# Kernel tuning notes

Measured on AMD Instinct MI355X. Metric: run time of the kernel, lower is better.

## Reference

```python
import jax, jax.numpy as jnp
import numpy as np

T, H, I = 8192, 2048, 768  # tokens, hidden_size, intermediate_size

def setup_inputs() -> dict:
    key = jax.random.key(0)
    k1, k2, k3, k4 = jax.random.split(key, 4)
    x = jax.random.normal(k1, (T, H), dtype=jnp.float32)
    # torch nn.Linear weight layout: [out_features, in_features]
    gate_w = jax.random.normal(k2, (I, H), dtype=jnp.float32) * (1.0 / np.sqrt(H))
    up_w = jax.random.normal(k3, (I, H), dtype=jnp.float32) * (1.0 / np.sqrt(H))
    down_w = jax.random.normal(k4, (H, I), dtype=jnp.float32) * (1.0 / np.sqrt(I))
    return {"x": x, "gate_w": gate_w, "up_w": up_w, "down_w": down_w}

def reference(x, gate_w, up_w, down_w):
    # fused SwiGLU MLP: down( silu(x @ gate^T) * (x @ up^T) )
    gate = jnp.einsum('th,ih->ti', x, gate_w)   # [T, I]
    up = jnp.einsum('th,ih->ti', x, up_w)       # [T, I]
    h = jax.nn.silu(gate) * up                   # [T, I]
    out = jnp.einsum('ti,hi->th', h, down_w)     # [T, H]
    return out
```

## Files before the change

kernel.cpp:

```cpp
#include <hip/hip_runtime.h>
#include <hip/hip_bf16.h>
#include <stdint.h>

#define T_DIM 8192
#define H_DIM 2048
#define I_DIM 768

typedef __bf16 bf16_t;
typedef bf16_t bf16x8 __attribute__((ext_vector_type(8)));
typedef bf16_t bf16x4 __attribute__((ext_vector_type(4)));
typedef float  f32x4  __attribute__((ext_vector_type(4)));

__device__ __forceinline__ void async_load16(const void* g, void* s) {
    __builtin_amdgcn_global_load_lds(
        (const __attribute__((address_space(1))) void*)g,
        (__attribute__((address_space(3))) void*)s, 16, 0, 0);
}

__global__ __launch_bounds__(256) void cvt_kernel(
    const float* __restrict__ X, const float* __restrict__ G,
    const float* __restrict__ U, const float* __restrict__ D,
    bf16_t* __restrict__ Xb, bf16_t* __restrict__ Gb,
    bf16_t* __restrict__ Ub, bf16_t* __restrict__ Db)
{
    const size_t N4X = (size_t)T_DIM * H_DIM / 4;
    const size_t N4W = (size_t)I_DIM * H_DIM / 4;
    const size_t total = N4X + 3 * N4W;
    for (size_t i = (size_t)blockIdx.x * blockDim.x + threadIdx.x; i < total;
         i += (size_t)gridDim.x * blockDim.x) {
        const float* s; bf16_t* d; size_t j = i;
        if (j < N4X) { s = X; d = Xb; }
        else {
            j -= N4X;
            if (j < N4W) { s = G; d = Gb; }
            else { j -= N4W;
                if (j < N4W) { s = U; d = Ub; }
                else { j -= N4W; s = D; d = Db; } }
        }
        float4 v = ((const float4*)s)[j];
        bf16x4 o;
        o[0] = (bf16_t)v.x; o[1] = (bf16_t)v.y; o[2] = (bf16_t)v.z; o[3] = (bf16_t)v.w;
        ((bf16x4*)d)[j] = o;
    }
}

__global__ __launch_bounds__(256) void gateup_kernel(
    const bf16_t* __restrict__ X,
    const bf16_t* __restrict__ Wg,
    const bf16_t* __restrict__ Wu,
    bf16_t* __restrict__ Hbuf)
{
    __shared__ __align__(16) bf16_t sA[128 * 32];
    __shared__ __align__(16) bf16_t sG[64 * 32];
    __shared__ __align__(16) bf16_t sU[64 * 32];

    const int tid   = threadIdx.x;
    const int lane  = tid & 63;
    const int wave  = tid >> 6;
    const int waveM = wave >> 1;
    const int waveN = wave & 1;
    const int quad  = lane >> 4;
    const int lrow  = lane & 15;

    const int blockM = blockIdx.x;
    const int blockN = blockIdx.y;

    f32x4 accG[4][2], accU[4][2];
#pragma unroll
    for (int i = 0; i < 4; i++)
#pragma unroll
        for (int j = 0; j < 2; j++) { accG[i][j] = (f32x4)(0.f); accU[i][j] = (f32x4)(0.f); }

    const int s0 = tid, s1 = tid + 256;
    const int rA0 = s0 >> 2, cA0 = (s0 & 3) * 8;
    const int rA1 = s1 >> 2, cA1 = (s1 & 3) * 8;
    const int rW  = tid >> 2, cW  = (tid & 3) * 8;

    const bf16_t* Ab = X  + (size_t)(blockM * 128) * H_DIM;
    const bf16_t* Gb = Wg + (size_t)(blockN * 64) * H_DIM;
    const bf16_t* Ub = Wu + (size_t)(blockN * 64) * H_DIM;

    for (int k0 = 0; k0 < H_DIM; k0 += 32) {
        async_load16(Ab + (size_t)rA0 * H_DIM + k0 + cA0, &sA[s0 * 8]);
        async_load16(Ab + (size_t)rA1 * H_DIM + k0 + cA1, &sA[s1 * 8]);
        async_load16(Gb + (size_t)rW  * H_DIM + k0 + cW,  &sG[tid * 8]);
        async_load16(Ub + (size_t)rW  * H_DIM + k0 + cW,  &sU[tid * 8]);
        __syncthreads();

        bf16x8 aF[4], gF[2], uF[2];
#pragma unroll
        for (int mi = 0; mi < 4; mi++) {
            int r = waveM * 64 + mi * 16 + lrow;
            aF[mi] = *(const bf16x8*)&sA[r * 32 + quad * 8];
        }
#pragma unroll
        for (int ni = 0; ni < 2; ni++) {
            int r = waveN * 32 + ni * 16 + lrow;
            gF[ni] = *(const bf16x8*)&sG[r * 32 + quad * 8];
            uF[ni] = *(const bf16x8*)&sU[r * 32 + quad * 8];
        }
        __syncthreads();

#pragma unroll
        for (int mi = 0; mi < 4; mi++)
#pragma unroll
            for (int ni = 0; ni < 2; ni++) {
                accG[mi][ni] = __builtin_amdgcn_mfma_f32_16x16x32_bf16(aF[mi], gF[ni], accG[mi][ni], 0, 0, 0);
                accU[mi][ni] = __builtin_amdgcn_mfma_f32_16x16x32_bf16(aF[mi], uF[ni], accU[mi][ni], 0, 0, 0);
            }
    }

#pragma unroll
    for (int mi = 0; mi < 4; mi++) {
#pragma unroll
        for (int ni = 0; ni < 2; ni++) {
#pragma unroll
            for (int r = 0; r < 4; r++) {
                int row = blockM * 128 + waveM * 64 + mi * 16 + quad * 4 + r;
                int col = blockN * 64 + waveN * 32 + ni * 16 + lrow;
                float g = accG[mi][ni][r];
                float u = accU[mi][ni][r];
                float h = (g / (1.f + __expf(-g))) * u;
                Hbuf[(size_t)row * I_DIM + col] = (bf16_t)h;
            }
        }
    }
}

__global__ __launch_bounds__(256) void down_kernel(
    const bf16_t* __restrict__ Hbuf,
    const bf16_t* __restrict__ Wd,
    float* __restrict__ Out)
{
    __shared__ __align__(16) bf16_t sA[128 * 32];
    __shared__ __align__(16) bf16_t sB[128 * 32];

    const int tid   = threadIdx.x;
    const int lane  = tid & 63;
    const int wave  = tid >> 6;
    const int waveM = wave >> 1;
    const int waveN = wave & 1;
    const int quad  = lane >> 4;
    const int lrow  = lane & 15;

    const int blockM = blockIdx.x;
    const int blockN = blockIdx.y;

    f32x4 acc[4][4];
#pragma unroll
    for (int i = 0; i < 4; i++)
#pragma unroll
        for (int j = 0; j < 4; j++) acc[i][j] = (f32x4)(0.f);

    const int s0 = tid, s1 = tid + 256;
    const int rA0 = s0 >> 2, cA0 = (s0 & 3) * 8;
    const int rA1 = s1 >> 2, cA1 = (s1 & 3) * 8;

    const bf16_t* Ab = Hbuf + (size_t)(blockM * 128) * I_DIM;
    const bf16_t* Bb = Wd   + (size_t)(blockN * 128) * I_DIM;

    for (int k0 = 0; k0 < I_DIM; k0 += 32) {
        async_load16(Ab + (size_t)rA0 * I_DIM + k0 + cA0, &sA[s0 * 8]);
        async_load16(Ab + (size_t)rA1 * I_DIM + k0 + cA1, &sA[s1 * 8]);
        async_load16(Bb + (size_t)rA0 * I_DIM + k0 + cA0, &sB[s0 * 8]);
        async_load16(Bb + (size_t)rA1 * I_DIM + k0 + cA1, &sB[s1 * 8]);
        __syncthreads();

        bf16x8 aF[4], bF[4];
#pragma unroll
        for (int mi = 0; mi < 4; mi++) {
            int r = waveM * 64 + mi * 16 + lrow;
            aF[mi] = *(const bf16x8*)&sA[r * 32 + quad * 8];
        }
#pragma unroll
        for (int ni = 0; ni < 4; ni++) {
            int r = waveN * 64 + ni * 16 + lrow;
            bF[ni] = *(const bf16x8*)&sB[r * 32 + quad * 8];
        }
        __syncthreads();

#pragma unroll
        for (int mi = 0; mi < 4; mi++)
#pragma unroll
            for (int ni = 0; ni < 4; ni++)
                acc[mi][ni] = __builtin_amdgcn_mfma_f32_16x16x32_bf16(aF[mi], bF[ni], acc[mi][ni], 0, 0, 0);
    }

#pragma unroll
    for (int mi = 0; mi < 4; mi++) {
#pragma unroll
        for (int ni = 0; ni < 4; ni++) {
#pragma unroll
            for (int r = 0; r < 4; r++) {
                int row = blockM * 128 + waveM * 64 + mi * 16 + quad * 4 + r;
                int col = blockN * 128 + waveN * 64 + ni * 16 + lrow;
                Out[(size_t)row * H_DIM + col] = acc[mi][ni][r];
            }
        }
    }
}

extern "C" void kernel_launch(void* const* d_in, const int* in_sizes, int n_in,
                              void* d_out, int out_size, void* d_ws, size_t ws_size,
                              hipStream_t stream) {
    const float* x  = (const float*)d_in[0];
    const float* gw = (const float*)d_in[1];
    const float* uw = (const float*)d_in[2];
    const float* dw = (const float*)d_in[3];
    float* out = (float*)d_out;

    bf16_t* xb = (bf16_t*)d_ws;
    bf16_t* gb = xb + (size_t)T_DIM * H_DIM;
    bf16_t* ub = gb + (size_t)I_DIM * H_DIM;
    bf16_t* db = ub + (size_t)I_DIM * H_DIM;
    bf16_t* hb = db + (size_t)I_DIM * H_DIM;

    cvt_kernel<<<2048, 256, 0, stream>>>(x, gw, uw, dw, xb, gb, ub, db);
    gateup_kernel<<<dim3(T_DIM / 128, I_DIM / 64), 256, 0, stream>>>(xb, gb, ub, hb);
    down_kernel<<<dim3(T_DIM / 128, H_DIM / 128), 256, 0, stream>>>(hb, db, out);
}
```

Before: 230.5 us.

## Double-buffer LDS tiles with prefetch and XOR-swizzle layout in both GEMMs

Both GEMM kernels now use two shared-memory buffers, issuing async global-to-LDS loads for the next K tile before computing the current one. Manual vmcnt waits and raw barriers replace the two __syncthreads per iteration. Global columns are XOR-swizzled into LDS and reads use matching precomputed offsets, to cut bank conflicts on fragment loads. This doubles LDS use per block, which may lower occupancy, and depends on the hand-written waitcnt ordering being correct.

```diff
diff --git a/kernel.cpp b/kernel.cpp
--- a/kernel.cpp
+++ b/kernel.cpp
@@ -44,15 +44,16 @@
     }
 }
 
+
 __global__ __launch_bounds__(256) void gateup_kernel(
     const bf16_t* __restrict__ X,
     const bf16_t* __restrict__ Wg,
     const bf16_t* __restrict__ Wu,
     bf16_t* __restrict__ Hbuf)
 {
-    __shared__ __align__(16) bf16_t sA[128 * 32];
-    __shared__ __align__(16) bf16_t sG[64 * 32];
-    __shared__ __align__(16) bf16_t sU[64 * 32];
+    __shared__ __align__(16) bf16_t sA[2][128 * 32];
+    __shared__ __align__(16) bf16_t sG[2][64 * 32];
+    __shared__ __align__(16) bf16_t sU[2][64 * 32];
 
     const int tid   = threadIdx.x;
     const int lane  = tid & 63;
@@ -72,34 +73,56 @@
         for (int j = 0; j < 2; j++) { accG[i][j] = (f32x4)(0.f); accU[i][j] = (f32x4)(0.f); }
 
     const int s0 = tid, s1 = tid + 256;
-    const int rA0 = s0 >> 2, cA0 = (s0 & 3) * 8;
-    const int rA1 = s1 >> 2, cA1 = (s1 & 3) * 8;
-    const int rW  = tid >> 2, cW  = (tid & 3) * 8;
+    const int rA0 = s0 >> 2, cA0 = (((s0 & 3) ^ ((rA0 >> 1) & 3)) * 8);
+    const int rA1 = s1 >> 2, cA1 = (((s1 & 3) ^ ((rA1 >> 1) & 3)) * 8);
+    const int rW  = tid >> 2, cW  = (((tid & 3) ^ ((rW >> 1) & 3)) * 8);
 
     const bf16_t* Ab = X  + (size_t)(blockM * 128) * H_DIM;
-    const bf16_t* Gb = Wg + (size_t)(blockN * 64) * H_DIM;
-    const bf16_t* Ub = Wu + (size_t)(blockN * 64) * H_DIM;
-
+    const bf16_t* Gw = Wg + (size_t)(blockN * 64) * H_DIM;
+    const bf16_t* Uw = Wu + (size_t)(blockN * 64) * H_DIM;
+
+    int aOff[4], wOff[2];
+#pragma unroll
+    for (int mi = 0; mi < 4; mi++) {
+        int r = waveM * 64 + mi * 16 + lrow;
+        aOff[mi] = r * 32 + ((quad ^ ((r >> 1) & 3)) * 8);
+    }
+#pragma unroll
+    for (int ni = 0; ni < 2; ni++) {
+        int r = waveN * 32 + ni * 16 + lrow;
+        wOff[ni] = r * 32 + ((quad ^ ((r >> 1) & 3)) * 8);
+    }
+
+    async_load16(Ab + (size_t)rA0 * H_DIM + cA0, &sA[0][s0 * 8]);
+    async_load16(Ab + (size_t)rA1 * H_DIM + cA1, &sA[0][s1 * 8]);
+    async_load16(Gw + (size_t)rW  * H_DIM + cW,  &sG[0][tid * 8]);
+    async_load16(Uw + (size_t)rW  * H_DIM + cW,  &sU[0][tid * 8]);
+
+    int cur = 0;
     for (int k0 = 0; k0 < H_DIM; k0 += 32) {
-        async_load16(Ab + (size_t)rA0 * H_DIM + k0 + cA0, &sA[s0 * 8]);
-        async_load16(Ab + (size_t)rA1 * H_DIM + k0 + cA1, &sA[s1 * 8]);
-        async_load16(Gb + (size_t)rW  * H_DIM + k0 + cW,  &sG[tid * 8]);
-        async_load16(Ub + (size_t)rW  * H_DIM + k0 + cW,  &sU[tid * 8]);
-        __syncthreads();
+        __builtin_amdgcn_s_barrier();
+        if (k0 + 32 < H_DIM) {
+            const int nxt = cur ^ 1;
+            async_load16(Ab + (size_t)rA0 * H_DIM + (k0 + 32) + cA0, &sA[nxt][s0 * 8]);
+            async_load16(Ab + (size_t)rA1 * H_DIM + (k0 + 32) + cA1, &sA[nxt][s1 * 8]);
+            async_load16(Gw + (size_t)rW  * H_DIM + (k0 + 32) + cW,  &sG[nxt][tid * 8]);
+            async_load16(Uw + (size_t)rW  * H_DIM + (k0 + 32) + cW,  &sU[nxt][tid * 8]);
+            asm volatile("s_waitcnt vmcnt(4)" ::: "memory");
+        } else {
+            asm volatile("s_waitcnt vmcnt(0)" ::: "memory");
+        }
+        __builtin_amdgcn_s_barrier();
+        asm volatile("" ::: "memory");
 
         bf16x8 aF[4], gF[2], uF[2];
 #pragma unroll
-        for (int mi = 0; mi < 4; mi++) {
-            int r = waveM * 64 + mi * 16 + lrow;
-            aF[mi] = *(const bf16x8*)&sA[r * 32 + quad * 8];
-        }
+        for (int mi = 0; mi < 4; mi++)
+            aF[mi] = *(const bf16x8*)&sA[cur][aOff[mi]];
 #pragma unroll
         for (int ni = 0; ni < 2; ni++) {
-            int r = waveN * 32 + ni * 16 + lrow;
-            gF[ni] = *(const bf16x8*)&sG[r * 32 + quad * 8];
-            uF[ni] = *(const bf16x8*)&sU[r * 32 + quad * 8];
-        }
-        __syncthreads();
+            gF[ni] = *(const bf16x8*)&sG[cur][wOff[ni]];
+            uF[ni] = *(const bf16x8*)&sU[cur][wOff[ni]];
+        }
 
 #pragma unroll
         for (int mi = 0; mi < 4; mi++)
@@ -108,6 +131,7 @@
                 accG[mi][ni] = __builtin_amdgcn_mfma_f32_16x16x32_bf16(aF[mi], gF[ni], accG[mi][ni], 0, 0, 0);
                 accU[mi][ni] = __builtin_amdgcn_mfma_f32_16x16x32_bf16(aF[mi], uF[ni], accU[mi][ni], 0, 0, 0);
             }
+        cur ^= 1;
     }
 
 #pragma unroll
@@ -132,8 +156,8 @@
     const bf16_t* __restrict__ Wd,
     float* __restrict__ Out)
 {
-    __shared__ __align__(16) bf16_t sA[128 * 32];
-    __shared__ __align__(16) bf16_t sB[128 * 32];
+    __shared__ __align__(16) bf16_t sA[2][128 * 32];
+    __shared__ __align__(16) bf16_t sB[2][128 * 32];
 
     const int tid   = threadIdx.x;
     const int lane  = tid & 63;
@@ -153,37 +177,59 @@
         for (int j = 0; j < 4; j++) acc[i][j] = (f32x4)(0.f);
 
     const int s0 = tid, s1 = tid + 256;
-    const int rA0 = s0 >> 2, cA0 = (s0 & 3) * 8;
-    const int rA1 = s1 >> 2, cA1 = (s1 & 3) * 8;
+    const int rA0 = s0 >> 2, cA0 = (((s0 & 3) ^ ((rA0 >> 1) & 3)) * 8);
+    const int rA1 = s1 >> 2, cA1 = (((s1 & 3) ^ ((rA1 >> 1) & 3)) * 8);
 
     const bf16_t* Ab = Hbuf + (size_t)(blockM * 128) * I_DIM;
     const bf16_t* Bb = Wd   + (size_t)(blockN * 128) * I_DIM;
 
+    int aOff[4], bOff[4];
+#pragma unroll
+    for (int mi = 0; mi < 4; mi++) {
+        int r = waveM * 64 + mi * 16 + lrow;
+        aOff[mi] = r * 32 + ((quad ^ ((r >> 1) & 3)) * 8);
+    }
+#pragma unroll
+    for (int ni = 0; ni < 4; ni++) {
+        int r = waveN * 64 + ni * 16 + lrow;
+        bOff[ni] = r * 32 + ((quad ^ ((r >> 1) & 3)) * 8);
+    }
+
+    async_load16(Ab + (size_t)rA0 * I_DIM + cA0, &sA[0][s0 * 8]);
+    async_load16(Ab + (size_t)rA1 * I_DIM + cA1, &sA[0][s1 * 8]);
+    async_load16(Bb + (size_t)rA0 * I_DIM + cA0, &sB[0][s0 * 8]);
+    async_load16(Bb + (size_t)rA1 * I_DIM + cA1, &sB[0][s1 * 8]);
+
+    int cur = 0;
     for (int k0 = 0; k0 < I_DIM; k0 += 32) {
-        async_load16(Ab + (size_t)rA0 * I_DIM + k0 + cA0, &sA[s0 * 8]);
-        async_load16(Ab + (size_t)rA1 * I_DIM + k0 + cA1, &sA[s1 * 8]);
-        async_load16(Bb + (size_t)rA0 * I_DIM + k0 + cA0, &sB[s0 * 8]);
-        async_load16(Bb + (size_t)rA1 * I_DIM + k0 + cA1, &sB[s1 * 8]);
-        __syncthreads();
+        __builtin_amdgcn_s_barrier();
+        if (k0 + 32 < I_DIM) {
+            const int nxt = cur ^ 1;
+            async_load16(Ab + (size_t)rA0 * I_DIM + (k0 + 32) + cA0, &sA[nxt][s0 * 8]);
+            async_load16(Ab + (size_t)rA1 * I_DIM + (k0 + 32) + cA1, &sA[nxt][s1 * 8]);
+            async_load16(Bb + (size_t)rA0 * I_DIM + (k0 + 32) + cA0, &sB[nxt][s0 * 8]);
+            async_load16(Bb + (size_t)rA1 * I_DIM + (k0 + 32) + cA1, &sB[nxt][s1 * 8]);
+            asm volatile("s_waitcnt vmcnt(4)" ::: "memory");
+        } else {
+            asm volatile("s_waitcnt vmcnt(0)" ::: "memory");
+        }
+        __builtin_amdgcn_s_barrier();
+        asm volatile("" ::: "memory");
 
         bf16x8 aF[4], bF[4];
 #pragma unroll
-        for (int mi = 0; mi < 4; mi++) {
-            int r = waveM * 64 + mi * 16 + lrow;
-            aF[mi] = *(const bf16x8*)&sA[r * 32 + quad * 8];
-        }
-#pragma unroll
-        for (int ni = 0; ni < 4; ni++) {
-            int r = waveN * 64 + ni * 16 + lrow;
-            bF[ni] = *(const bf16x8*)&sB[r * 32 + quad * 8];
-        }
-        __syncthreads();
+        for (int mi = 0; mi < 4; mi++)
+            aF[mi] = *(const bf16x8*)&sA[cur][aOff[mi]];
+#pragma unroll
+        for (int ni = 0; ni < 4; ni++)
+            bF[ni] = *(const bf16x8*)&sB[cur][bOff[ni]];
 
 #pragma unroll
         for (int mi = 0; mi < 4; mi++)
 #pragma unroll
             for (int ni = 0; ni < 4; ni++)
                 acc[mi][ni] = __builtin_amdgcn_mfma_f32_16x16x32_bf16(aF[mi], bF[ni], acc[mi][ni], 0, 0, 0);
+        cur ^= 1;
     }
 
 #pragma unroll
```

After: 251.2 us. +9.0%, slower.

## Double K-tile depth to 64 with XOR-swizzled LDS layout in both GEMMs

Applied to the files above, without the earlier changes.

Both GEMM kernels now stage 64-wide K slices per iteration instead of 32, halving the number of barrier pairs and load rounds. The LDS layout uses an XOR swizzle of the 16-byte chunk index by row, so fragment reads avoid bank conflicts. Each staged tile feeds two MFMA sub-steps. The convert kernel also handles 8 elements per thread with 16-byte bf16 stores, and down_kernel gets a launch-bounds occupancy hint. The larger LDS footprint may reduce the number of resident blocks.

```diff
diff --git a/kernel.cpp b/kernel.cpp
--- a/kernel.cpp
+++ b/kernel.cpp
@@ -23,26 +23,29 @@
     bf16_t* __restrict__ Xb, bf16_t* __restrict__ Gb,
     bf16_t* __restrict__ Ub, bf16_t* __restrict__ Db)
 {
-    const size_t N4X = (size_t)T_DIM * H_DIM / 4;
-    const size_t N4W = (size_t)I_DIM * H_DIM / 4;
-    const size_t total = N4X + 3 * N4W;
+    const size_t N8X = (size_t)T_DIM * H_DIM / 8;
+    const size_t N8W = (size_t)I_DIM * H_DIM / 8;
+    const size_t total = N8X + 3 * N8W;
     for (size_t i = (size_t)blockIdx.x * blockDim.x + threadIdx.x; i < total;
          i += (size_t)gridDim.x * blockDim.x) {
         const float* s; bf16_t* d; size_t j = i;
-        if (j < N4X) { s = X; d = Xb; }
+        if (j < N8X) { s = X; d = Xb; }
         else {
-            j -= N4X;
-            if (j < N4W) { s = G; d = Gb; }
-            else { j -= N4W;
-                if (j < N4W) { s = U; d = Ub; }
-                else { j -= N4W; s = D; d = Db; } }
-        }
-        float4 v = ((const float4*)s)[j];
-        bf16x4 o;
-        o[0] = (bf16_t)v.x; o[1] = (bf16_t)v.y; o[2] = (bf16_t)v.z; o[3] = (bf16_t)v.w;
-        ((bf16x4*)d)[j] = o;
-    }
-}
+            j -= N8X;
+            if (j < N8W) { s = G; d = Gb; }
+            else { j -= N8W;
+                if (j < N8W) { s = U; d = Ub; }
+                else { j -= N8W; s = D; d = Db; } }
+        }
+        float4 v0 = ((const float4*)s)[2 * j];
+        float4 v1 = ((const float4*)s)[2 * j + 1];
+        bf16x8 o;
+        o[0] = (bf16_t)v0.x; o[1] = (bf16_t)v0.y; o[2] = (bf16_t)v0.z; o[3] = (bf16_t)v0.w;
+        o[4] = (bf16_t)v1.x; o[5] = (bf16_t)v1.y; o[6] = (bf16_t)v1.z; o[7] = (bf16_t)v1.w;
+        ((bf16x8*)d)[j] = o;
+    }
+}
+
 
 __global__ __launch_bounds__(256) void gateup_kernel(
     const bf16_t* __restrict__ X,
@@ -50,9 +53,9 @@
     const bf16_t* __restrict__ Wu,
     bf16_t* __restrict__ Hbuf)
 {
-    __shared__ __align__(16) bf16_t sA[128 * 32];
-    __shared__ __align__(16) bf16_t sG[64 * 32];
-    __shared__ __align__(16) bf16_t sU[64 * 32];
+    __shared__ __align__(16) bf16_t sA[128 * 64];
+    __shared__ __align__(16) bf16_t sG[64 * 64];
+    __shared__ __align__(16) bf16_t sU[64 * 64];
 
     const int tid   = threadIdx.x;
     const int lane  = tid & 63;
@@ -71,43 +74,72 @@
 #pragma unroll
         for (int j = 0; j < 2; j++) { accG[i][j] = (f32x4)(0.f); accU[i][j] = (f32x4)(0.f); }
 
-    const int s0 = tid, s1 = tid + 256;
-    const int rA0 = s0 >> 2, cA0 = (s0 & 3) * 8;
-    const int rA1 = s1 >> 2, cA1 = (s1 & 3) * 8;
-    const int rW  = tid >> 2, cW  = (tid & 3) * 8;
-
     const bf16_t* Ab = X  + (size_t)(blockM * 128) * H_DIM;
-    const bf16_t* Gb = Wg + (size_t)(blockN * 64) * H_DIM;
-    const bf16_t* Ub = Wu + (size_t)(blockN * 64) * H_DIM;
-
-    for (int k0 = 0; k0 < H_DIM; k0 += 32) {
-        async_load16(Ab + (size_t)rA0 * H_DIM + k0 + cA0, &sA[s0 * 8]);
-        async_load16(Ab + (size_t)rA1 * H_DIM + k0 + cA1, &sA[s1 * 8]);
-        async_load16(Gb + (size_t)rW  * H_DIM + k0 + cW,  &sG[tid * 8]);
-        async_load16(Ub + (size_t)rW  * H_DIM + k0 + cW,  &sU[tid * 8]);
-        __syncthreads();
-
-        bf16x8 aF[4], gF[2], uF[2];
-#pragma unroll
-        for (int mi = 0; mi < 4; mi++) {
-            int r = waveM * 64 + mi * 16 + lrow;
-            aF[mi] = *(const bf16x8*)&sA[r * 32 + quad * 8];
-        }
-#pragma unroll
-        for (int ni = 0; ni < 2; ni++) {
-            int r = waveN * 32 + ni * 16 + lrow;
-            gF[ni] = *(const bf16x8*)&sG[r * 32 + quad * 8];
-            uF[ni] = *(const bf16x8*)&sU[r * 32 + quad * 8];
-        }
-        __syncthreads();
-
-#pragma unroll
-        for (int mi = 0; mi < 4; mi++)
+    const bf16_t* Gw = Wg + (size_t)(blockN * 64) * H_DIM;
+    const bf16_t* Uw = Wu + (size_t)(blockN * 64) * H_DIM;
+
+    int aRow[4], aCol[4];
+#pragma unroll
+    for (int i = 0; i < 4; i++) {
+        int s = tid + 256 * i;
+        aRow[i] = s >> 3;
+        aCol[i] = ((s & 7) ^ ((s >> 3) & 7)) * 8;
+    }
+    int wRow[2], wCol[2];
+#pragma unroll
+    for (int i = 0; i < 2; i++) {
+        int s = tid + 256 * i;
+        wRow[i] = s >> 3;
+        wCol[i] = ((s & 7) ^ ((s >> 3) & 7)) * 8;
+    }
+
+    int aOff[4], wOff[2];
+#pragma unroll
+    for (int mi = 0; mi < 4; mi++) {
+        int r = waveM * 64 + mi * 16 + lrow;
+        aOff[mi] = r * 64 + ((quad ^ (r & 7)) * 8);
+    }
+#pragma unroll
+    for (int ni = 0; ni < 2; ni++) {
+        int r = waveN * 32 + ni * 16 + lrow;
+        wOff[ni] = r * 64 + ((quad ^ (r & 7)) * 8);
+    }
+
+    for (int k0 = 0; k0 < H_DIM; k0 += 64) {
+#pragma unroll
+        for (int i = 0; i < 4; i++)
+            async_load16(Ab + (size_t)aRow[i] * H_DIM + k0 + aCol[i],
+                         &sA[(tid + 256 * i) * 8]);
+#pragma unroll
+        for (int i = 0; i < 2; i++) {
+            async_load16(Gw + (size_t)wRow[i] * H_DIM + k0 + wCol[i],
+                         &sG[(tid + 256 * i) * 8]);
+            async_load16(Uw + (size_t)wRow[i] * H_DIM + k0 + wCol[i],
+                         &sU[(tid + 256 * i) * 8]);
+        }
+        __syncthreads();
+
+#pragma unroll
+        for (int kk = 0; kk < 2; kk++) {
+            const int kx = kk * 32;
+            bf16x8 aF[4], gF[2], uF[2];
+#pragma unroll
+            for (int mi = 0; mi < 4; mi++)
+                aF[mi] = *(const bf16x8*)&sA[aOff[mi] ^ kx];
 #pragma unroll
             for (int ni = 0; ni < 2; ni++) {
-                accG[mi][ni] = __builtin_amdgcn_mfma_f32_16x16x32_bf16(aF[mi], gF[ni], accG[mi][ni], 0, 0, 0);
-                accU[mi][ni] = __builtin_amdgcn_mfma_f32_16x16x32_bf16(aF[mi], uF[ni], accU[mi][ni], 0, 0, 0);
+                gF[ni] = *(const bf16x8*)&sG[wOff[ni] ^ kx];
+                uF[ni] = *(const bf16x8*)&sU[wOff[ni] ^ kx];
             }
+#pragma unroll
+            for (int mi = 0; mi < 4; mi++)
+#pragma unroll
+                for (int ni = 0; ni < 2; ni++) {
+                    accG[mi][ni] = __builtin_amdgcn_mfma_f32_16x16x32_bf16(aF[mi], gF[ni], accG[mi][ni], 0, 0, 0);
+                    accU[mi][ni] = __builtin_amdgcn_mfma_f32_16x16x32_bf16(aF[mi], uF[ni], accU[mi][ni], 0, 0, 0);
+                }
+        }
+        __syncthreads();
     }
 
 #pragma unroll
@@ -127,13 +159,13 @@
     }
 }
 
-__global__ __launch_bounds__(256) void down_kernel(
+__global__ __launch_bounds__(256, 4) void down_kernel(
     const bf16_t* __restrict__ Hbuf,
     const bf16_t* __restrict__ Wd,
     float* __restrict__ Out)
 {
-    __shared__ __align__(16) bf16_t sA[128 * 32];
-    __shared__ __align__(16) bf16_t sB[128 * 32];
+    __shared__ __align__(16) bf16_t sA[128 * 64];
+    __shared__ __align__(16) bf16_t sB[128 * 64];
 
     const int tid   = threadIdx.x;
     const int lane  = tid & 63;
@@ -152,38 +184,56 @@
 #pragma unroll
         for (int j = 0; j < 4; j++) acc[i][j] = (f32x4)(0.f);
 
-    const int s0 = tid, s1 = tid + 256;
-    const int rA0 = s0 >> 2, cA0 = (s0 & 3) * 8;
-    const int rA1 = s1 >> 2, cA1 = (s1 & 3) * 8;
-
     const bf16_t* Ab = Hbuf + (size_t)(blockM * 128) * I_DIM;
     const bf16_t* Bb = Wd   + (size_t)(blockN * 128) * I_DIM;
 
-    for (int k0 = 0; k0 < I_DIM; k0 += 32) {
-        async_load16(Ab + (size_t)rA0 * I_DIM + k0 + cA0, &sA[s0 * 8]);
-        async_load16(Ab + (size_t)rA1 * I_DIM + k0 + cA1, &sA[s1 * 8]);
-        async_load16(Bb + (size_t)rA0 * I_DIM + k0 + cA0, &sB[s0 * 8]);
-        async_load16(Bb + (size_t)rA1 * I_DIM + k0 + cA1, &sB[s1 * 8]);
-        __syncthreads();
-
-        bf16x8 aF[4], bF[4];
-#pragma unroll
-        for (int mi = 0; mi < 4; mi++) {
-            int r = waveM * 64 + mi * 16 + lrow;
-            aF[mi] = *(const bf16x8*)&sA[r * 32 + quad * 8];
-        }
-#pragma unroll
-        for (int ni = 0; ni < 4; ni++) {
-            int r = waveN * 64 + ni * 16 + lrow;
-            bF[ni] = *(const bf16x8*)&sB[r * 32 + quad * 8];
-        }
-        __syncthreads();
-
-#pragma unroll
-        for (int mi = 0; mi < 4; mi++)
+    int gRow[4], gCol[4];
+#pragma unroll
+    for (int i = 0; i < 4; i++) {
+        int s = tid + 256 * i;
+        gRow[i] = s >> 3;
+        gCol[i] = ((s & 7) ^ ((s >> 3) & 7)) * 8;
+    }
+
+    int aOff[4], bOff[4];
+#pragma unroll
+    for (int mi = 0; mi < 4; mi++) {
+        int r = waveM * 64 + mi * 16 + lrow;
+        aOff[mi] = r * 64 + ((quad ^ (r & 7)) * 8);
+    }
+#pragma unroll
+    for (int ni = 0; ni < 4; ni++) {
+        int r = waveN * 64 + ni * 16 + lrow;
+        bOff[ni] = r * 64 + ((quad ^ (r & 7)) * 8);
+    }
+
+    for (int k0 = 0; k0 < I_DIM; k0 += 64) {
+#pragma unroll
+        for (int i = 0; i < 4; i++) {
+            async_load16(Ab + (size_t)gRow[i] * I_DIM + k0 + gCol[i],
+                         &sA[(tid + 256 * i) * 8]);
+            async_load16(Bb + (size_t)gRow[i] * I_DIM + k0 + gCol[i],
+                         &sB[(tid + 256 * i) * 8]);
+        }
+        __syncthreads();
+
+#pragma unroll
+        for (int kk = 0; kk < 2; kk++) {
+            const int kx = kk * 32;
+            bf16x8 aF[4], bF[4];
+#pragma unroll
+            for (int mi = 0; mi < 4; mi++)
+                aF[mi] = *(const bf16x8*)&sA[aOff[mi] ^ kx];
 #pragma unroll
             for (int ni = 0; ni < 4; ni++)
-                acc[mi][ni] = __builtin_amdgcn_mfma_f32_16x16x32_bf16(aF[mi], bF[ni], acc[mi][ni], 0, 0, 0);
+                bF[ni] = *(const bf16x8*)&sB[bOff[ni] ^ kx];
+#pragma unroll
+            for (int mi = 0; mi < 4; mi++)
+#pragma unroll
+                for (int ni = 0; ni < 4; ni++)
+                    acc[mi][ni] = __builtin_amdgcn_mfma_f32_16x16x32_bf16(aF[mi], bF[ni], acc[mi][ni], 0, 0, 0);
+        }
+        __syncthreads();
     }
 
 #pragma unroll
```

Result: slower. 238.4 us (+3.4%).
